# Kernel optimization log

Measured on AMD Instinct MI355X. Metric: run time of the kernel, lower is better.

## Reference

```python
import jax
import jax.numpy as jnp
from jax import lax
import numpy as np

VOCAB = 50000
EMB = 32
HID = 32
LAYERS = 4
BATCH = 8192
SEQ = 111


def setup_inputs() -> dict:
    key = jax.random.key(0)
    ks = jax.random.split(key, 12)
    s = 0.1
    x = jax.random.randint(ks[0], (BATCH, SEQ), 0, VOCAB, dtype=jnp.int64 if jax.config.read('jax_enable_x64') else jnp.int32)
    emb = jax.random.normal(ks[1], (VOCAB, EMB), jnp.float32) * s
    # stacked per-layer LSTM weights; layer-0 input dim == EMB == HID so stacking is valid
    Wih = jax.random.normal(ks[2], (LAYERS, 4 * HID, EMB), jnp.float32) * s
    Whh = jax.random.normal(ks[3], (LAYERS, 4 * HID, HID), jnp.float32) * s
    bih = jax.random.normal(ks[4], (LAYERS, 4 * HID), jnp.float32) * s
    bhh = jax.random.normal(ks[5], (LAYERS, 4 * HID), jnp.float32) * s
    Wa = jax.random.normal(ks[6], (HID, 1), jnp.float32) * s
    ba = jax.random.normal(ks[7], (1,), jnp.float32) * s
    W1 = jax.random.normal(ks[8], (HID, 32), jnp.float32) * s
    b1 = jax.random.normal(ks[9], (32,), jnp.float32) * s
    W2 = jax.random.normal(ks[10], (32, 3), jnp.float32) * s
    b2 = jax.random.normal(ks[11], (3,), jnp.float32) * s
    return {"x": x, "emb": emb, "Wih": Wih, "Whh": Whh, "bih": bih, "bhh": bhh,
            "Wa": Wa, "ba": ba, "W1": W1, "b1": b1, "W2": W2, "b2": b2}


def _lstm_layer(x, Wih, Whh, bih, bhh):
    # x: [B, T, D] -> [B, T, H]; PyTorch gate order: i, f, g, o
    B = x.shape[0]
    H = Whh.shape[1]
    # precompute the input contribution for all timesteps (one big GEMM)
    xg = jnp.einsum('btd,gd->btg', x, Wih) + bih + bhh  # [B, T, 4H]

    def step(carry, xg_t):
        h, c = carry
        z = xg_t + h @ Whh.T  # [B, 4H]
        i, f, g, o = jnp.split(z, 4, axis=-1)
        c = jax.nn.sigmoid(f) * c + jax.nn.sigmoid(i) * jnp.tanh(g)
        h = jax.nn.sigmoid(o) * jnp.tanh(c)
        return (h, c), h

    init = (jnp.zeros((B, H), x.dtype), jnp.zeros((B, H), x.dtype))
    _, hs = lax.scan(step, init, jnp.swapaxes(xg, 0, 1))  # hs: [T, B, H]
    return jnp.swapaxes(hs, 0, 1)


def reference(x, emb, Wih, Whh, bih, bhh, Wa, ba, W1, b1, W2, b2):
    h = emb[x]  # [B, T, E]
    for l in range(Wih.shape[0]):  # fixed 4 layers
        h = _lstm_layer(h, Wih[l], Whh[l], bih[l], bhh[l])
    scores = h @ Wa + ba                       # [B, T, 1]
    attn = jax.nn.softmax(scores, axis=1)      # softmax over time
    context = jnp.sum(h * attn, axis=1)        # [B, H]
    hid = jnp.tanh(context @ W1 + b1)          # dropout is identity at eval
    return hid @ W2 + b2                       # [B, 3]
```

## Files before the change

### kernel.cpp

```cpp
#include <hip/hip_runtime.h>

#define TSEQ 111
#define L2E 1.44269504088896340736f
#define TWO_L2E 2.88539008177792680472f

using f32x4  = __attribute__((ext_vector_type(4))) float;
using short8 = __attribute__((ext_vector_type(8))) short;

union FragU { unsigned u[4]; uint4 v; short8 s; };

__device__ __forceinline__ float fexp2(float x) { return __builtin_amdgcn_exp2f(x); }
__device__ __forceinline__ float frcp(float x)  { return __builtin_amdgcn_rcpf(x); }
__device__ __forceinline__ float tanh2(float zs) { return 1.f - 2.f * frcp(1.f + fexp2(zs + zs)); }

__device__ __forceinline__ unsigned rnd_bf16(float w) {
  unsigned u = __float_as_uint(w);
  return (u + 0x7fffu + ((u >> 16) & 1u)) >> 16;
}
__device__ __forceinline__ unsigned cvtpk(float a, float b) {
  unsigned r;
  asm("v_cvt_pk_bf16_f32 %0, %1, %2" : "=v"(r) : "v"(a), "v"(b));
  return r;
}

__global__ __launch_bounds__(512, 4) void lstm_fused(
    const int* __restrict__ x, const float* __restrict__ emb,
    const float* __restrict__ Wih, const float* __restrict__ Whh,
    const float* __restrict__ bih, const float* __restrict__ bhh,
    const float* __restrict__ Wa, const float* __restrict__ W1,
    const float* __restrict__ b1, const float* __restrict__ W2,
    const float* __restrict__ b2, float* __restrict__ out)
{
  __shared__ __align__(16) unsigned short hb[2 * 5 * 512];

  const int tid  = threadIdx.x;
  const int wv2  = tid >> 6;
  const int l    = wv2 >> 1;
  const int hf   = wv2 & 1;
  const int lane = tid & 63;
  const int c    = lane & 15;
  const int q    = lane >> 4;
  const int gc   = (c & 3) ^ (c >> 2);
  const int rowbase = blockIdx.x * 16;
  const int xrow = (rowbase + c) * TSEQ;

  const int rdOff = c * 32 + ((q ^ gc) << 3);
  const int u     = hf * 16 + c;
  const int uhi   = (u >> 3);
  const int ulo   = (u & 7);

  FragU wihf[4], whhf[4];
#pragma unroll
  for (int g = 0; g < 4; ++g) {
    const float sj = (g == 2) ? TWO_L2E : -L2E;
    const int j = 2 * g + hf;
    const float* srcI = Wih + l * 4096 + (16 * j + c) * 32 + 8 * q;
    const float* srcH = Whh + l * 4096 + (16 * j + c) * 32 + 8 * q;
#pragma unroll
    for (int p = 0; p < 4; ++p) {
      wihf[g].u[p] = rnd_bf16(srcI[2 * p] * sj) | (rnd_bf16(srcI[2 * p + 1] * sj) << 16);
      whhf[g].u[p] = rnd_bf16(srcH[2 * p] * sj) | (rnd_bf16(srcH[2 * p + 1] * sj) << 16);
    }
  }
  f32x4 bvv[4];
#pragma unroll
  for (int g = 0; g < 4; ++g) {
    const float sj = (g == 2) ? TWO_L2E : -L2E;
    const int j = 2 * g + hf;
    float b = (bih[l * 128 + 16 * j + c] + bhh[l * 128 + 16 * j + c]) * sj;
    bvv[g][0] = b; bvv[g][1] = b; bvv[g][2] = b; bvv[g][3] = b;
  }

  FragU wafh, wafl;
#pragma unroll
  for (int p = 0; p < 4; ++p) { wafh.u[p] = 0u; wafl.u[p] = 0u; }
  if (l == 3 && c == 0) {
#pragma unroll
    for (int p = 0; p < 4; ++p) {
      const int k0 = 8 * q + 2 * p;
      float w0 = Wa[k0] * L2E, w1 = Wa[k0 + 1] * L2E;
      unsigned h0 = rnd_bf16(w0), h1b = rnd_bf16(w1);
      wafh.u[p] = h0 | (h1b << 16);
      float l0 = w0 - __uint_as_float(h0 << 16);
      float l1 = w1 - __uint_as_float(h1b << 16);
      wafl.u[p] = rnd_bf16(l0) | (rnd_bf16(l1) << 16);
    }
  }

  float cs[4], mr[4], sr[4], cx[4], h1[4];
#pragma unroll
  for (int e = 0; e < 4; ++e) {
    cs[e] = 0.f; mr[e] = -1e30f; sr[e] = 0.f; cx[e] = 0.f; h1[e] = 0.f;
  }

  for (int i = tid; i < 2 * 5 * 512 / 2; i += 512) ((unsigned*)hb)[i] = 0u;
  __syncthreads();

  float4 embR = make_float4(0.f, 0.f, 0.f, 0.f);
  int idx2 = 0;
  const int embWrOff = c * 32 + ((((hf << 1) + (q >> 1)) ^ gc) << 3) + ((q & 1) << 2);
  if (l == 0) {
    int i0 = x[xrow];
    float4 a = *(const float4*)(emb + i0 * 32 + hf * 16 + 4 * q);
    *(uint2*)(hb + (1 * 5 + 0) * 512 + embWrOff) = make_uint2(cvtpk(a.x, a.y), cvtpk(a.z, a.w));
    int i1 = x[xrow + 1];
    embR = *(const float4*)(emb + i1 * 32 + hf * 16 + 4 * q);
    idx2 = x[xrow + 2];
  }
  __syncthreads();

  for (int s = 0; s < TSEQ + 4; ++s) {
    const int t = s - l;
    const bool active = ((unsigned)t < (unsigned)TSEQ);
    const int rp = (s + 1) & 1;
    const int wp = s & 1;

    if (l == 0) {
      if (t + 1 < TSEQ)
        *(uint2*)(hb + (wp * 5 + 0) * 512 + embWrOff) =
            make_uint2(cvtpk(embR.x, embR.y), cvtpk(embR.z, embR.w));
      if (t + 2 < TSEQ) embR = *(const float4*)(emb + idx2 * 32 + hf * 16 + 4 * q);
      if (t + 3 < TSEQ) idx2 = x[xrow + t + 3];
    }

    const bool rdF = active || (l == 3 && s == TSEQ + 3);
    FragU fi, fh;
    if (active) fi.v = *(const uint4*)(hb + (rp * 5 + l) * 512 + rdOff);
    if (rdF)    fh.v = *(const uint4*)(hb + (rp * 5 + l + 1) * 512 + rdOff);

    f32x4 acc[4];
    if (active) {
#pragma unroll
      for (int g = 0; g < 4; ++g) {
        acc[g] = __builtin_amdgcn_mfma_f32_16x16x32_bf16(fi.s, wihf[g].s, bvv[g], 0, 0, 0);
        acc[g] = __builtin_amdgcn_mfma_f32_16x16x32_bf16(fh.s, whhf[g].s, acc[g], 0, 0, 0);
      }
    }

    if (l == 3 && s >= 4) {
      f32x4 sacc = __builtin_amdgcn_mfma_f32_16x16x32_bf16(
          fh.s, wafh.s, (f32x4){0.f, 0.f, 0.f, 0.f}, 0, 0, 0);
      sacc = __builtin_amdgcn_mfma_f32_16x16x32_bf16(fh.s, wafl.s, sacc, 0, 0, 0);
      float pf[4];
#pragma unroll
      for (int e = 0; e < 4; ++e)
        pf[e] = __int_as_float(
            __builtin_amdgcn_ds_swizzle(__float_as_int(sacc[e]), 0x0010));
#pragma unroll
      for (int e = 0; e < 4; ++e) {
        float mn = fmaxf(mr[e], pf[e]);
        float sc = fexp2(mr[e] - mn);
        float pr = fexp2(pf[e] - mn);
        sr[e] = sr[e] * sc + pr;
        cx[e] = cx[e] * sc + pr * h1[e];
        mr[e] = mn;
      }
    }

    if (active) {
      float hv[4];
#pragma unroll
      for (int e = 0; e < 4; ++e) {
        float a_ = fexp2(acc[0][e]);
        float m_ = fexp2(acc[1][e]);
        float b_ = fexp2(acc[2][e]);
        float p_ = fexp2(acc[3][e]);
        float P  = (1.f + a_) * (1.f + b_);
        float M1 = 1.f + m_;
        float cn = (cs[e] * P + (b_ - 1.f) * M1) * frcp(M1 * P);
        cs[e] = cn;
        float qv = fexp2(fminf(cn * TWO_L2E, 80.f));
        hv[e] = (qv - 1.f) * frcp((1.f + p_) * (1.f + qv));
      }

      {
        unsigned short* ob = hb + (wp * 5 + l + 1) * 512;
        unsigned u01 = cvtpk(hv[0], hv[1]);
        unsigned u23 = cvtpk(hv[2], hv[3]);
        const int r0 = 4 * q;
        ob[(r0 + 0) * 32 + (((uhi ^ (0 ^ q)) << 3) | ulo)] = (unsigned short)(u01 & 0xffffu);
        ob[(r0 + 1) * 32 + (((uhi ^ (1 ^ q)) << 3) | ulo)] = (unsigned short)(u01 >> 16);
        ob[(r0 + 2) * 32 + (((uhi ^ (2 ^ q)) << 3) | ulo)] = (unsigned short)(u23 & 0xffffu);
        ob[(r0 + 3) * 32 + (((uhi ^ (3 ^ q)) << 3) | ulo)] = (unsigned short)(u23 >> 16);
      }

      if (l == 3) {
#pragma unroll
        for (int e = 0; e < 4; ++e) h1[e] = hv[e];
      }
    }

    asm volatile("s_waitcnt lgkmcnt(0)\n\ts_barrier" ::: "memory");
  }

  __syncthreads();

  float* cb = (float*)hb;
  if (l == 3) {
#pragma unroll
    for (int e = 0; e < 4; ++e) {
      const int r = 4 * q + e;
      float inv = frcp(sr[e]);
      cb[r * 33 + hf * 16 + c] = cx[e] * inv;
    }
  }
  __syncthreads();
  if (wv2 != 6) return;

  float a0[4], a1[4];
  {
    float bb0 = b1[c], bb1 = b1[c + 16];
#pragma unroll
    for (int e = 0; e < 4; ++e) { a0[e] = bb0; a1[e] = bb1; }
    for (int j = 0; j < 32; ++j) {
      float w0 = W1[j * 32 + c];
      float w1 = W1[j * 32 + c + 16];
#pragma unroll
      for (int e = 0; e < 4; ++e) {
        float cr = cb[(4 * q + e) * 33 + j];
        a0[e] = fmaf(cr, w0, a0[e]);
        a1[e] = fmaf(cr, w1, a1[e]);
      }
    }
  }
  float o0[4], o1[4], o2[4];
  {
    float w20 = W2[c * 3 + 0], w21 = W2[c * 3 + 1], w22 = W2[c * 3 + 2];
    float w30 = W2[(c + 16) * 3 + 0], w31 = W2[(c + 16) * 3 + 1], w32 = W2[(c + 16) * 3 + 2];
#pragma unroll
    for (int e = 0; e < 4; ++e) {
      float h0 = tanh2(a0[e] * L2E);
      float hB = tanh2(a1[e] * L2E);
      o0[e] = h0 * w20 + hB * w30;
      o1[e] = h0 * w21 + hB * w31;
      o2[e] = h0 * w22 + hB * w32;
    }
  }
#pragma unroll
  for (int mk = 1; mk <= 8; mk <<= 1) {
#pragma unroll
    for (int e = 0; e < 4; ++e) {
      o0[e] += __shfl_xor(o0[e], mk, 64);
      o1[e] += __shfl_xor(o1[e], mk, 64);
      o2[e] += __shfl_xor(o2[e], mk, 64);
    }
  }
  if (c < 3) {
    float bb = b2[c];
#pragma unroll
    for (int e = 0; e < 4; ++e) {
      float v = (c == 0) ? o0[e] : ((c == 1) ? o1[e] : o2[e]);
      out[(rowbase + 4 * q + e) * 3 + c] = v + bb;
    }
  }
}

extern "C" void kernel_launch(void* const* d_in, const int* in_sizes, int n_in,
                              void* d_out, int out_size, void* d_ws, size_t ws_size,
                              hipStream_t stream) {
  const int*   x   = (const int*)d_in[0];
  const float* emb = (const float*)d_in[1];
  const float* Wih = (const float*)d_in[2];
  const float* Whh = (const float*)d_in[3];
  const float* bih = (const float*)d_in[4];
  const float* bhh = (const float*)d_in[5];
  const float* Wa  = (const float*)d_in[6];
  const float* W1  = (const float*)d_in[8];
  const float* b1  = (const float*)d_in[9];
  const float* W2  = (const float*)d_in[10];
  const float* b2  = (const float*)d_in[11];
  float* out = (float*)d_out;

  lstm_fused<<<512, 512, 0, stream>>>(x, emb, Wih, Whh, bih, bhh, Wa, W1, b1, W2, b2, out);
}
```

Before: 176.7 us.

## Spread embedding gather across all waves and move attention to layer-1 waves

The embedding gather and bf16 store are now spread across all eight waves at one element per thread, instead of being done by layer-0 waves as float4 loads. The attention-score MFMA and online softmax move from the layer-3 waves, which sit on the critical path, to the layer-1 waves. Those waves read the final hidden state from shared memory and use a transposed MFMA so each lane holds a single score. The wave index is made uniform with readfirstlane and the time loop is unrolled by two. This balances per-wave work in the lockstep barrier loop, at the cost of an extra LDS read per step and scattered scalar embedding loads from every wave.

```diff
diff --git a/kernel.cpp b/kernel.cpp
--- a/kernel.cpp
+++ b/kernel.cpp
@@ -34,20 +34,25 @@
   __shared__ __align__(16) unsigned short hb[2 * 5 * 512];
 
   const int tid  = threadIdx.x;
-  const int wv2  = tid >> 6;
-  const int l    = wv2 >> 1;
-  const int hf   = wv2 & 1;
+  const int wvu  = __builtin_amdgcn_readfirstlane(tid) >> 6;
+  const int l    = wvu >> 1;
+  const int hf   = wvu & 1;
   const int lane = tid & 63;
   const int c    = lane & 15;
   const int q    = lane >> 4;
-  const int gc   = (c & 3) ^ (c >> 2);
+  const int gcc  = (c & 3) ^ (c >> 2);
   const int rowbase = blockIdx.x * 16;
-  const int xrow = (rowbase + c) * TSEQ;
-
-  const int rdOff = c * 32 + ((q ^ gc) << 3);
+
+  const int rdOff = c * 32 + ((q ^ gcc) << 3);
   const int u     = hf * 16 + c;
   const int uhi   = (u >> 3);
   const int ulo   = (u & 7);
+
+  const int srow  = 2 * wvu + (lane >> 5);
+  const int scol  = lane & 31;
+  const int sgc   = (srow & 3) ^ (srow >> 2);
+  const int sOff  = srow * 32 + ((((scol >> 3) ^ sgc)) << 3) + (scol & 7);
+  const int sxrow = (rowbase + srow) * TSEQ;
 
   FragU wihf[4], whhf[4];
 #pragma unroll
@@ -71,93 +76,68 @@
     bvv[g][0] = b; bvv[g][1] = b; bvv[g][2] = b; bvv[g][3] = b;
   }
 
-  FragU wafh, wafl;
-#pragma unroll
-  for (int p = 0; p < 4; ++p) { wafh.u[p] = 0u; wafl.u[p] = 0u; }
-  if (l == 3 && c == 0) {
+  FragU wahA, walA;
+#pragma unroll
+  for (int p = 0; p < 4; ++p) { wahA.u[p] = 0u; walA.u[p] = 0u; }
+  if (l == 1) {
 #pragma unroll
     for (int p = 0; p < 4; ++p) {
       const int k0 = 8 * q + 2 * p;
       float w0 = Wa[k0] * L2E, w1 = Wa[k0 + 1] * L2E;
       unsigned h0 = rnd_bf16(w0), h1b = rnd_bf16(w1);
-      wafh.u[p] = h0 | (h1b << 16);
+      wahA.u[p] = h0 | (h1b << 16);
       float l0 = w0 - __uint_as_float(h0 << 16);
       float l1 = w1 - __uint_as_float(h1b << 16);
-      wafl.u[p] = rnd_bf16(l0) | (rnd_bf16(l1) << 16);
-    }
-  }
-
-  float cs[4], mr[4], sr[4], cx[4], h1[4];
-#pragma unroll
-  for (int e = 0; e < 4; ++e) {
-    cs[e] = 0.f; mr[e] = -1e30f; sr[e] = 0.f; cx[e] = 0.f; h1[e] = 0.f;
-  }
+      walA.u[p] = rnd_bf16(l0) | (rnd_bf16(l1) << 16);
+    }
+  }
+
+  float cs[4];
+#pragma unroll
+  for (int e = 0; e < 4; ++e) cs[e] = 0.f;
+  float mr = -1e30f, sr = 0.f, cx[4];
+#pragma unroll
+  for (int e = 0; e < 4; ++e) cx[e] = 0.f;
 
   for (int i = tid; i < 2 * 5 * 512 / 2; i += 512) ((unsigned*)hb)[i] = 0u;
   __syncthreads();
 
-  float4 embR = make_float4(0.f, 0.f, 0.f, 0.f);
-  int idx2 = 0;
-  const int embWrOff = c * 32 + ((((hf << 1) + (q >> 1)) ^ gc) << 3) + ((q & 1) << 2);
-  if (l == 0) {
-    int i0 = x[xrow];
-    float4 a = *(const float4*)(emb + i0 * 32 + hf * 16 + 4 * q);
-    *(uint2*)(hb + (1 * 5 + 0) * 512 + embWrOff) = make_uint2(cvtpk(a.x, a.y), cvtpk(a.z, a.w));
-    int i1 = x[xrow + 1];
-    embR = *(const float4*)(emb + i1 * 32 + hf * 16 + 4 * q);
-    idx2 = x[xrow + 2];
-  }
-  __syncthreads();
-
+  {
+    int i0 = x[sxrow];
+    float e0 = emb[i0 * 32 + scol];
+    hb[(1 * 5 + 0) * 512 + sOff] = (unsigned short)rnd_bf16(e0);
+  }
+  float embv = emb[x[sxrow + 1] * 32 + scol];
+  int idxn = x[sxrow + 2];
+  __syncthreads();
+
+#pragma unroll 2
   for (int s = 0; s < TSEQ + 4; ++s) {
     const int t = s - l;
     const bool active = ((unsigned)t < (unsigned)TSEQ);
     const int rp = (s + 1) & 1;
     const int wp = s & 1;
 
-    if (l == 0) {
-      if (t + 1 < TSEQ)
-        *(uint2*)(hb + (wp * 5 + 0) * 512 + embWrOff) =
-            make_uint2(cvtpk(embR.x, embR.y), cvtpk(embR.z, embR.w));
-      if (t + 2 < TSEQ) embR = *(const float4*)(emb + idx2 * 32 + hf * 16 + 4 * q);
-      if (t + 3 < TSEQ) idx2 = x[xrow + t + 3];
-    }
-
-    const bool rdF = active || (l == 3 && s == TSEQ + 3);
-    FragU fi, fh;
-    if (active) fi.v = *(const uint4*)(hb + (rp * 5 + l) * 512 + rdOff);
-    if (rdF)    fh.v = *(const uint4*)(hb + (rp * 5 + l + 1) * 512 + rdOff);
-
-    f32x4 acc[4];
+    if (s + 1 < TSEQ) hb[(wp * 5 + 0) * 512 + sOff] = (unsigned short)rnd_bf16(embv);
+    if (s + 2 < TSEQ) embv = emb[idxn * 32 + scol];
+    if (s + 3 < TSEQ) idxn = x[sxrow + s + 3];
+
+    FragU fi, fh, f3;
     if (active) {
+      fi.v = *(const uint4*)(hb + (rp * 5 + l) * 512 + rdOff);
+      fh.v = *(const uint4*)(hb + (rp * 5 + l + 1) * 512 + rdOff);
+    }
+    const bool doAtt = (l == 1) && (s >= 4);
+    if (doAtt) f3.v = *(const uint4*)(hb + (rp * 5 + 4) * 512 + rdOff);
+
+    if (active) {
+      f32x4 acc[4];
 #pragma unroll
       for (int g = 0; g < 4; ++g) {
         acc[g] = __builtin_amdgcn_mfma_f32_16x16x32_bf16(fi.s, wihf[g].s, bvv[g], 0, 0, 0);
         acc[g] = __builtin_amdgcn_mfma_f32_16x16x32_bf16(fh.s, whhf[g].s, acc[g], 0, 0, 0);
       }
-    }
-
-    if (l == 3 && s >= 4) {
-      f32x4 sacc = __builtin_amdgcn_mfma_f32_16x16x32_bf16(
-          fh.s, wafh.s, (f32x4){0.f, 0.f, 0.f, 0.f}, 0, 0, 0);
-      sacc = __builtin_amdgcn_mfma_f32_16x16x32_bf16(fh.s, wafl.s, sacc, 0, 0, 0);
-      float pf[4];
-#pragma unroll
-      for (int e = 0; e < 4; ++e)
-        pf[e] = __int_as_float(
-            __builtin_amdgcn_ds_swizzle(__float_as_int(sacc[e]), 0x0010));
-#pragma unroll
-      for (int e = 0; e < 4; ++e) {
-        float mn = fmaxf(mr[e], pf[e]);
-        float sc = fexp2(mr[e] - mn);
-        float pr = fexp2(pf[e] - mn);
-        sr[e] = sr[e] * sc + pr;
-        cx[e] = cx[e] * sc + pr * h1[e];
-        mr[e] = mn;
-      }
-    }
-
-    if (active) {
+
       float hv[4];
 #pragma unroll
       for (int e = 0; e < 4; ++e) {
@@ -183,11 +163,26 @@
         ob[(r0 + 2) * 32 + (((uhi ^ (2 ^ q)) << 3) | ulo)] = (unsigned short)(u23 & 0xffffu);
         ob[(r0 + 3) * 32 + (((uhi ^ (3 ^ q)) << 3) | ulo)] = (unsigned short)(u23 >> 16);
       }
-
-      if (l == 3) {
-#pragma unroll
-        for (int e = 0; e < 4; ++e) h1[e] = hv[e];
-      }
+    }
+
+    if (doAtt) {
+      f32x4 z = {0.f, 0.f, 0.f, 0.f};
+      f32x4 sacc = __builtin_amdgcn_mfma_f32_16x16x32_bf16(wahA.s, f3.s, z, 0, 0, 0);
+      sacc = __builtin_amdgcn_mfma_f32_16x16x32_bf16(walA.s, f3.s, sacc, 0, 0, 0);
+      float pf = sacc[0];
+      float mn = fmaxf(mr, pf);
+      float sc = fexp2(mr - mn);
+      float pr = fexp2(pf - mn);
+      sr = sr * sc + pr;
+#pragma unroll
+      for (int p = 0; p < 2; ++p) {
+        unsigned w = f3.u[2 * hf + p];
+        float vlo = __uint_as_float(w << 16);
+        float vhi = __uint_as_float(w & 0xffff0000u);
+        cx[2 * p]     = cx[2 * p]     * sc + pr * vlo;
+        cx[2 * p + 1] = cx[2 * p + 1] * sc + pr * vhi;
+      }
+      mr = mn;
     }
 
     asm volatile("s_waitcnt lgkmcnt(0)\n\ts_barrier" ::: "memory");
@@ -196,16 +191,14 @@
   __syncthreads();
 
   float* cb = (float*)hb;
-  if (l == 3) {
-#pragma unroll
-    for (int e = 0; e < 4; ++e) {
-      const int r = 4 * q + e;
-      float inv = frcp(sr[e]);
-      cb[r * 33 + hf * 16 + c] = cx[e] * inv;
-    }
-  }
-  __syncthreads();
-  if (wv2 != 6) return;
+  if (l == 1) {
+    float inv = frcp(sr);
+#pragma unroll
+    for (int e = 0; e < 4; ++e)
+      cb[c * 33 + 8 * q + 4 * hf + e] = cx[e] * inv;
+  }
+  __syncthreads();
+  if (wvu != 6) return;
 
   float a0[4], a1[4];
   {
```

Result: faster. 167.5 us (-5.2%).
